# Performance work log

Measured on AMD Instinct MI355X. Metric: run time of the kernel, lower is better.

The kernel has to match this reference:

```python
import jax, jax.numpy as jnp
import numpy as np

N_ATOMS = 8192
N_EDGES = 262144
N_MOL = 128
F = 128
R = 20
CUTOFF = 5.0
L = 3
EPS = 1e-8


def setup_inputs() -> dict:
    key = jax.random.key(0)
    ks = jax.random.split(key, 20)
    sc = 0.05  # weight init scale for numerical stability
    inp = {
        "z": jax.random.randint(ks[0], (N_ATOMS,), 0, 100, dtype=jnp.int32),
        "pos": jax.random.uniform(ks[1], (N_ATOMS, 3), dtype=jnp.float32),
        "edge_src": jax.random.randint(ks[2], (N_EDGES,), 0, N_ATOMS, dtype=jnp.int32),
        "edge_dst": jax.random.randint(ks[3], (N_EDGES,), 0, N_ATOMS, dtype=jnp.int32),
        "mol_idx": jnp.sort(jax.random.randint(ks[4], (N_ATOMS,), 0, N_MOL, dtype=jnp.int32)),
        "embed": jax.random.normal(ks[5], (100, F), dtype=jnp.float32) * sc,
        "msg_w1": jax.random.normal(ks[6], (L, F, F), dtype=jnp.float32) * sc,
        "msg_b1": jnp.zeros((L, F), jnp.float32),
        "msg_w2": jax.random.normal(ks[7], (L, F, 3 * F), dtype=jnp.float32) * sc,
        "msg_b2": jnp.zeros((L, 3 * F), jnp.float32),
        "rbf_w": jax.random.normal(ks[8], (L, R, 3 * F), dtype=jnp.float32) * sc,
        "rbf_b": jnp.zeros((L, 3 * F), jnp.float32),
        "upd_u": jax.random.normal(ks[9], (L, F, F), dtype=jnp.float32) * sc,
        "upd_v": jax.random.normal(ks[10], (L, F, F), dtype=jnp.float32) * sc,
        "upd_a1": jax.random.normal(ks[11], (L, 2 * F, F), dtype=jnp.float32) * sc,
        "upd_a1b": jnp.zeros((L, F), jnp.float32),
        "upd_a2": jax.random.normal(ks[12], (L, F, 3 * F), dtype=jnp.float32) * sc,
        "upd_a2b": jnp.zeros((L, 3 * F), jnp.float32),
        "out_w1": jax.random.normal(ks[13], (F, F), dtype=jnp.float32) * sc,
        "out_b1": jnp.zeros((F,), jnp.float32),
        "out_w2": jax.random.normal(ks[14], (F, 1), dtype=jnp.float32) * sc,
        "out_b2": jnp.zeros((1,), jnp.float32),
    }
    return inp


def _painn_forward(z, pos, edge_src, edge_dst, mol_idx, embed,
                   msg_w1, msg_b1, msg_w2, msg_b2, rbf_w, rbf_b,
                   upd_u, upd_v, upd_a1, upd_a1b, upd_a2, upd_a2b,
                   out_w1, out_b1, out_w2, out_b2):
    n = z.shape[0]
    s = embed[z]                                  # [N,F]
    v = jnp.zeros((n, 3, F), s.dtype)             # [N,3,F]

    rij = pos[edge_dst] - pos[edge_src]           # [E,3]
    d = jnp.sqrt(jnp.sum(rij * rij, axis=-1) + EPS)  # [E]
    unit = rij / d[:, None]                       # [E,3]
    freq = jnp.arange(1, R + 1, dtype=s.dtype) * (jnp.pi / CUTOFF)
    rbf = jnp.sin(d[:, None] * freq[None, :]) / d[:, None]          # [E,R]
    fc = 0.5 * (jnp.cos(jnp.pi * d / CUTOFF) + 1.0) * (d < CUTOFF)  # [E]

    for l in range(L):
        # --- message block ---
        phi = jax.nn.silu(s @ msg_w1[l] + msg_b1[l]) @ msg_w2[l] + msg_b2[l]  # [N,3F]
        wfilt = (rbf @ rbf_w[l] + rbf_b[l]) * fc[:, None]                      # [E,3F]
        m = phi[edge_src] * wfilt                                              # [E,3F]
        ds_e, dvv, dvs = m[:, :F], m[:, F:2 * F], m[:, 2 * F:]
        ds = jax.ops.segment_sum(ds_e, edge_dst, num_segments=n)
        dv_e = v[edge_src] * dvv[:, None, :] + unit[:, :, None] * dvs[:, None, :]  # [E,3,F]
        dv = jax.ops.segment_sum(dv_e, edge_dst, num_segments=n)
        s = s + ds
        v = v + dv
        # --- update block ---
        uv = jnp.einsum('ncf,fg->ncg', v, upd_u[l])   # [N,3,F]
        vv = jnp.einsum('ncf,fg->ncg', v, upd_v[l])   # [N,3,F]
        vv_norm = jnp.sqrt(jnp.sum(vv * vv, axis=1) + EPS)  # [N,F]
        a = jax.nn.silu(jnp.concatenate([s, vv_norm], axis=-1) @ upd_a1[l] + upd_a1b[l])
        a = a @ upd_a2[l] + upd_a2b[l]                # [N,3F]
        a_vv, a_sv, a_ss = a[:, :F], a[:, F:2 * F], a[:, 2 * F:]
        s = s + a_ss + a_sv * jnp.sum(uv * vv, axis=1)
        v = v + a_vv[:, None, :] * uv

    atom_out = jax.nn.silu(s @ out_w1 + out_b1) @ out_w2 + out_b2  # [N,1]
    return jax.ops.segment_sum(atom_out, mol_idx, num_segments=N_MOL)  # [M,1]


def reference(z, pos, edge_src, edge_dst, mol_idx, embed,
              msg_w1, msg_b1, msg_w2, msg_b2, rbf_w, rbf_b,
              upd_u, upd_v, upd_a1, upd_a1b, upd_a2, upd_a2b,
              out_w1, out_b1, out_w2, out_b2):
    return _painn_forward(z, pos, edge_src, edge_dst, mol_idx, embed,
                          msg_w1, msg_b1, msg_w2, msg_b2, rbf_w, rbf_b,
                          upd_u, upd_v, upd_a1, upd_a1b, upd_a2, upd_a2b,
                          out_w1, out_b1, out_w2, out_b2)
```

## Files before the change

### kernel.cpp

```cpp
#include <hip/hip_runtime.h>
#include <hip/hip_bf16.h>
#include <math.h>

#define N_ATOMS 8192
#define N_EDGES 262144
#define N_MOL   128
#define FDIM    128
#define RDIM    20
#define LLAYERS 3
#define CUTOFF  5.0f
#define EPSV    1e-8f
#define PI_F    3.14159265358979323846f

typedef __attribute__((ext_vector_type(8))) short bf16x8;
typedef __attribute__((ext_vector_type(4))) float f32x4;

#define VPLANE 1048576

__device__ __forceinline__ ushort f2bf(float x) {
    uint b = __float_as_uint(x);
    return (ushort)((b + 0x7fffu + ((b >> 16) & 1u)) >> 16);
}

__global__ void k_wconv(const float* __restrict__ w1, const float* __restrict__ w2,
                        const float* __restrict__ uu, const float* __restrict__ uvw,
                        const float* __restrict__ a1, const float* __restrict__ a2,
                        const float* __restrict__ ow1, ushort* __restrict__ WT) {
    int i = blockIdx.x * 256 + threadIdx.x;
    float v;
    if (i < 49152) {
        int idx = i; int l = idx >> 14; idx &= 16383;
        int n = idx >> 7, k = idx & 127;
        v = w1[l*16384 + k*128 + n];
    } else if (i < 196608) {
        int idx = i - 49152; int l = idx / 49152; idx -= l * 49152;
        int n = idx >> 7, k = idx & 127;
        v = w2[l*49152 + k*384 + n];
    } else if (i < 294912) {
        int idx = i - 196608; int l = idx >> 15; idx &= 32767;
        int n = idx >> 7, k = idx & 127;
        v = (n < 128) ? uu[l*16384 + k*128 + n] : uvw[l*16384 + k*128 + (n-128)];
    } else if (i < 393216) {
        int idx = i - 294912; int l = idx >> 15; idx &= 32767;
        int n = idx >> 8, k = idx & 255;
        v = a1[l*32768 + k*128 + n];
    } else if (i < 540672) {
        int idx = i - 393216; int l = idx / 49152; idx -= l * 49152;
        int n = idx >> 7, k = idx & 127;
        v = a2[l*49152 + k*384 + n];
    } else {
        int idx = i - 540672;
        int n = idx >> 7, k = idx & 127;
        v = ow1[k*128 + n];
    }
    WT[i] = f2bf(v);
}

__global__ void k_embed(const int* __restrict__ z, const float* __restrict__ embed,
                        float* __restrict__ S, ushort* __restrict__ SBF) {
    int i = blockIdx.x * 256 + threadIdx.x;
    int a = i >> 7, k = i & 127;
    float v = embed[(size_t)z[a] * FDIM + k];
    S[i] = v; SBF[i] = f2bf(v);
}

__global__ void k_hist(const int* __restrict__ edst, int* __restrict__ CNT) {
    int e = blockIdx.x * 256 + threadIdx.x;
    if (e < N_EDGES) atomicAdd(&CNT[edst[e]], 1);
}

__global__ __launch_bounds__(1024) void k_scan(const int* __restrict__ CNT,
                                               int* __restrict__ OFF, int* __restrict__ CUR) {
    __shared__ int part[1024];
    int t = threadIdx.x;
    int loc[8];
    int run = 0;
    #pragma unroll
    for (int i = 0; i < 8; i++) { int c = CNT[t*8 + i]; loc[i] = run; run += c; }
    part[t] = run;
    __syncthreads();
    for (int off = 1; off < 1024; off <<= 1) {
        int v = 0;
        if (t >= off) v = part[t - off];
        __syncthreads();
        part[t] += v;
        __syncthreads();
    }
    int ebase = (t > 0) ? part[t-1] : 0;
    #pragma unroll
    for (int i = 0; i < 8; i++) { int o = ebase + loc[i]; OFF[t*8+i] = o; CUR[t*8+i] = o; }
    if (t == 1023) OFF[8192] = part[1023];
}

__global__ void k_edges(const float* __restrict__ pos, const int* __restrict__ esrc,
                        const int* __restrict__ edst, int* __restrict__ CUR,
                        float* __restrict__ UNITFC, int* __restrict__ SRCS) {
    int e = blockIdx.x * 256 + threadIdx.x;
    if (e >= N_EDGES) return;
    int s = esrc[e], d = edst[e];
    int p = atomicAdd(&CUR[d], 1);
    float rx = pos[d*3+0] - pos[s*3+0];
    float ry = pos[d*3+1] - pos[s*3+1];
    float rz = pos[d*3+2] - pos[s*3+2];
    float dd = sqrtf(rx*rx + ry*ry + rz*rz + EPSV);
    float inv = 1.0f / dd;
    float4 u4; u4.x = rx*inv; u4.y = ry*inv; u4.z = rz*inv; u4.w = dd;
    *(float4*)&UNITFC[(size_t)p*4] = u4;
    SRCS[p] = s;
}

__global__ __launch_bounds__(256) void k_msg(
    const ushort* __restrict__ SBF, const ushort* __restrict__ W1T, const float* __restrict__ b1,
    const ushort* __restrict__ W2T, const float* __restrict__ b2, ushort* __restrict__ PHIB)
{
    int tid = threadIdx.x;
    int w = tid >> 6, l = tid & 63;
    int bm = blockIdx.x * 16;
    int lrow = l & 15, lk = (l >> 4) * 8;
    __shared__ ushort Hs[16][136];

    f32x4 acc[2] = {{0.f,0.f,0.f,0.f},{0.f,0.f,0.f,0.f}};
    #pragma unroll
    for (int k0 = 0; k0 < 128; k0 += 32) {
        bf16x8 af = *(const bf16x8*)&SBF[(size_t)(bm + lrow)*128 + k0 + lk];
        #pragma unroll
        for (int t = 0; t < 2; t++) {
            int n = (2*w + t)*16 + lrow;
            bf16x8 bf = *(const bf16x8*)&W1T[(size_t)n*128 + k0 + lk];
            acc[t] = __builtin_amdgcn_mfma_f32_16x16x32_bf16(af, bf, acc[t], 0, 0, 0);
        }
    }
    #pragma unroll
    for (int t = 0; t < 2; t++) {
        int col = (2*w + t)*16 + lrow;
        float bv = b1[col];
        #pragma unroll
        for (int j = 0; j < 4; j++) {
            int row = (l >> 4)*4 + j;
            float val = acc[t][j] + bv;
            val = val / (1.0f + __expf(-val));
            Hs[row][col] = f2bf(val);
        }
    }
    __syncthreads();

    f32x4 acc2[6];
    #pragma unroll
    for (int t = 0; t < 6; t++) acc2[t] = (f32x4){0.f,0.f,0.f,0.f};
    #pragma unroll
    for (int k0 = 0; k0 < 128; k0 += 32) {
        bf16x8 af = *(const bf16x8*)&Hs[lrow][k0 + lk];
        #pragma unroll
        for (int t = 0; t < 6; t++) {
            int n = (6*w + t)*16 + lrow;
            bf16x8 bf = *(const bf16x8*)&W2T[(size_t)n*128 + k0 + lk];
            acc2[t] = __builtin_amdgcn_mfma_f32_16x16x32_bf16(af, bf, acc2[t], 0, 0, 0);
        }
    }
    #pragma unroll
    for (int t = 0; t < 6; t++) {
        int col = (6*w + t)*16 + lrow;
        float bv = b2[col];
        #pragma unroll
        for (int j = 0; j < 4; j++) {
            int row = bm + (l >> 4)*4 + j;
            PHIB[(size_t)row*384 + col] = f2bf(acc2[t][j] + bv);
        }
    }
}

template<bool L0>
__global__ __launch_bounds__(192) void k_aggregate(
    const ushort* __restrict__ PHIB, const ushort* __restrict__ VBFA,
    float* __restrict__ S, ushort* __restrict__ SBF,
    float* __restrict__ V, ushort* __restrict__ VBFB,
    const float* __restrict__ UNITFC,
    const int* __restrict__ SRCS, const int* __restrict__ OFF,
    const float* __restrict__ rbfw, const float* __restrict__ rbfb)
{
    int a = blockIdx.x;
    int tid = threadIdx.x;
    int g = tid >> 6;
    int c0 = 2 * (tid & 63);

    float2 w[RDIM];
    const float* wc = rbfw + g*128 + c0;
    #pragma unroll
    for (int r = 0; r < RDIM; r++) { w[r].x = wc[r*384]; w[r].y = wc[r*384 + 1]; }
    float2 bb; bb.x = rbfb[g*128 + c0]; bb.y = rbfb[g*128 + c0 + 1];

    __shared__ int sSrc[64];
    __shared__ float4 sRBF[320];
    __shared__ float4 sUFC[64];
    __shared__ float avs[3][128];
    float* sRBFf = (float*)sRBF;

    int beg = OFF[a], end = OFF[a + 1];
    float2 d; d.x = 0.f; d.y = 0.f;
    float2 A0, A1, A2v;
    A0.x=A0.y=A1.x=A1.y=A2v.x=A2v.y=0.f;

    for (int p0 = beg; p0 < end; p0 += 64) {
        int n = end - p0; if (n > 64) n = 64;
        __syncthreads();
        if (tid < n) {
            sSrc[tid] = SRCS[p0 + tid];
            float4 u4 = *(const float4*)(UNITFC + (size_t)(p0 + tid) * 4);
            float dd = u4.w;
            u4.w = (dd < CUTOFF) ? 0.5f * (__cosf(dd * (PI_F / CUTOFF)) + 1.0f) : 0.0f;
            sUFC[tid] = u4;
        }
        for (int i = tid; i < n * RDIM; i += 192) {
            int e = i / RDIM, r = i - e * RDIM;
            float dd = UNITFC[(size_t)(p0 + e) * 4 + 3];
            sRBFf[i] = __sinf(dd * (float)(r + 1) * (PI_F / CUTOFF)) / dd;
        }
        __syncthreads();

        if (L0 && g == 1) continue;

        uint phA[4], u0A[4], u1A[4], u2A[4];
        uint phB[4], u0B[4], u1B[4], u2B[4];

        auto grpLoad = [&](int base, uint* ph, uint* u0, uint* u1, uint* u2) {
            #pragma unroll
            for (int j = 0; j < 4; j++) {
                int q = base + j;
                int src = sSrc[(q < n) ? q : 0];
                size_t pb = (size_t)src * 128;
                ph[j] = *(const uint*)&PHIB[(size_t)src*384 + g*128 + c0];
                if (!L0 && g == 1) {
                    u0[j] = *(const uint*)&VBFA[pb + c0];
                    u1[j] = *(const uint*)&VBFA[pb + VPLANE + c0];
                    u2[j] = *(const uint*)&VBFA[pb + 2*VPLANE + c0];
                }
            }
        };
        grpLoad(0, phA, u0A, u1A, u2A);
        for (int q0 = 0; q0 < n; q0 += 4) {
            if (q0 + 4 < n) grpLoad(q0 + 4, phB, u0B, u1B, u2B);
            #pragma unroll
            for (int j = 0; j < 4; j++) {
                int q = q0 + j;
                if (q >= n) break;
                float4 r0 = sRBF[q*5+0], r1 = sRBF[q*5+1], r2 = sRBF[q*5+2],
                       r3 = sRBF[q*5+3], r4 = sRBF[q*5+4];
                float4 ufc = sUFC[q];
                float2 f = bb;
                f.x += r0.x*w[0].x;   f.y += r0.x*w[0].y;
                f.x += r0.y*w[1].x;   f.y += r0.y*w[1].y;
                f.x += r0.z*w[2].x;   f.y += r0.z*w[2].y;
                f.x += r0.w*w[3].x;   f.y += r0.w*w[3].y;
                f.x += r1.x*w[4].x;   f.y += r1.x*w[4].y;
                f.x += r1.y*w[5].x;   f.y += r1.y*w[5].y;
                f.x += r1.z*w[6].x;   f.y += r1.z*w[6].y;
                f.x += r1.w*w[7].x;   f.y += r1.w*w[7].y;
                f.x += r2.x*w[8].x;   f.y += r2.x*w[8].y;
                f.x += r2.y*w[9].x;   f.y += r2.y*w[9].y;
                f.x += r2.z*w[10].x;  f.y += r2.z*w[10].y;
                f.x += r2.w*w[11].x;  f.y += r2.w*w[11].y;
                f.x += r3.x*w[12].x;  f.y += r3.x*w[12].y;
                f.x += r3.y*w[13].x;  f.y += r3.y*w[13].y;
                f.x += r3.z*w[14].x;  f.y += r3.z*w[14].y;
                f.x += r3.w*w[15].x;  f.y += r3.w*w[15].y;
                f.x += r4.x*w[16].x;  f.y += r4.x*w[16].y;
                f.x += r4.y*w[17].x;  f.y += r4.y*w[17].y;
                f.x += r4.z*w[18].x;  f.y += r4.z*w[18].y;
                f.x += r4.w*w[19].x;  f.y += r4.w*w[19].y;
                uint up = phA[j];
                float m0 = __uint_as_float(up << 16)         * (f.x * ufc.w);
                float m1 = __uint_as_float(up & 0xffff0000u) * (f.y * ufc.w);
                if (g == 0) {
                    d.x += m0; d.y += m1;
                } else if (g == 1) {
                    A0.x  += __uint_as_float(u0A[j] << 16)         * m0;
                    A0.y  += __uint_as_float(u0A[j] & 0xffff0000u) * m1;
                    A1.x  += __uint_as_float(u1A[j] << 16)         * m0;
                    A1.y  += __uint_as_float(u1A[j] & 0xffff0000u) * m1;
                    A2v.x += __uint_as_float(u2A[j] << 16)         * m0;
                    A2v.y += __uint_as_float(u2A[j] & 0xffff0000u) * m1;
                } else {
                    A0.x  += ufc.x * m0; A0.y  += ufc.x * m1;
                    A1.x  += ufc.y * m0; A1.y  += ufc.y * m1;
                    A2v.x += ufc.z * m0; A2v.y += ufc.z * m1;
                }
            }
            #pragma unroll
            for (int j = 0; j < 4; j++) {
                phA[j] = phB[j]; u0A[j] = u0B[j]; u1A[j] = u1B[j]; u2A[j] = u2B[j];
            }
        }
    }

    if (g == 1) {
        avs[0][c0] = A0.x;  avs[0][c0+1] = A0.y;
        avs[1][c0] = A1.x;  avs[1][c0+1] = A1.y;
        avs[2][c0] = A2v.x; avs[2][c0+1] = A2v.y;
    }
    __syncthreads();
    if (g == 0) {
        size_t sb = (size_t)a*128 + c0;
        float2 s2 = *(float2*)&S[sb];
        s2.x += d.x; s2.y += d.y;
        *(float2*)&S[sb] = s2;
        SBF[sb] = f2bf(s2.x); SBF[sb+1] = f2bf(s2.y);
    } else if (g == 2) {
        float own0[3] = {A0.x, A1.x, A2v.x};
        float own1[3] = {A0.y, A1.y, A2v.y};
        #pragma unroll
        for (int c = 0; c < 3; c++) {
            size_t vb = (size_t)c*VPLANE + (size_t)a*128 + c0;
            float2 vi;
            if (L0) { vi.x = 0.f; vi.y = 0.f; }
            else    vi = *(const float2*)&V[vb];
            vi.x += avs[c][c0]     + own0[c];
            vi.y += avs[c][c0 + 1] + own1[c];
            *(float2*)&V[vb] = vi;
            VBFB[vb] = f2bf(vi.x); VBFB[vb+1] = f2bf(vi.y);
        }
    }
}

__global__ __launch_bounds__(256) void k_upd(
    const ushort* __restrict__ VBFB, const ushort* __restrict__ UVT,
    const ushort* __restrict__ SBF_in,
    const ushort* __restrict__ A1T, const float* __restrict__ a1b,
    const ushort* __restrict__ A2T, const float* __restrict__ a2b,
    float* __restrict__ S, ushort* __restrict__ SBF,
    float* __restrict__ V, ushort* __restrict__ VBFA)
{
    int tid = threadIdx.x;
    int w = tid >> 6, l = tid & 63;
    int bm = blockIdx.x * 16;
    int lrow = l & 15, lk = (l >> 4) * 8;
    __shared__ ushort sVVN[16][136];
    __shared__ ushort Hs[16][136];

    f32x4 au[3][2], av[3][2];
    #pragma unroll
    for (int c = 0; c < 3; c++)
        #pragma unroll
        for (int t = 0; t < 2; t++) {
            au[c][t] = (f32x4){0.f,0.f,0.f,0.f};
            av[c][t] = (f32x4){0.f,0.f,0.f,0.f};
        }
    #pragma unroll
    for (int k0 = 0; k0 < 128; k0 += 32) {
        bf16x8 af[3];
        #pragma unroll
        for (int c = 0; c < 3; c++)
            af[c] = *(const bf16x8*)&VBFB[(size_t)c*VPLANE + (size_t)(bm + lrow)*128 + k0 + lk];
        #pragma unroll
        for (int t = 0; t < 2; t++) {
            int nu = (2*w + t)*16 + lrow;
            bf16x8 bu = *(const bf16x8*)&UVT[(size_t)nu*128 + k0 + lk];
            bf16x8 bv = *(const bf16x8*)&UVT[(size_t)(nu + 128)*128 + k0 + lk];
            #pragma unroll
            for (int c = 0; c < 3; c++) {
                au[c][t] = __builtin_amdgcn_mfma_f32_16x16x32_bf16(af[c], bu, au[c][t], 0, 0, 0);
                av[c][t] = __builtin_amdgcn_mfma_f32_16x16x32_bf16(af[c], bv, av[c][t], 0, 0, 0);
            }
        }
    }
    float dotr[2][4], uvr[3][2][4];
    #pragma unroll
    for (int t = 0; t < 2; t++) {
        int k = (2*w + t)*16 + lrow;
        #pragma unroll
        for (int j = 0; j < 4; j++) {
            int row = (l >> 4)*4 + j;
            float u0 = au[0][t][j], u1 = au[1][t][j], u2 = au[2][t][j];
            float v0 = av[0][t][j], v1 = av[1][t][j], v2 = av[2][t][j];
            uvr[0][t][j] = u0; uvr[1][t][j] = u1; uvr[2][t][j] = u2;
            dotr[t][j] = u0*v0 + u1*v1 + u2*v2;
            sVVN[row][k] = f2bf(sqrtf(v0*v0 + v1*v1 + v2*v2 + EPSV));
        }
    }
    __syncthreads();

    f32x4 acc[2] = {{0.f,0.f,0.f,0.f},{0.f,0.f,0.f,0.f}};
    #pragma unroll
    for (int k0 = 0; k0 < 256; k0 += 32) {
        bf16x8 af;
        if (k0 < 128) af = *(const bf16x8*)&SBF_in[(size_t)(bm + lrow)*128 + k0 + lk];
        else          af = *(const bf16x8*)&sVVN[lrow][k0 + lk - 128];
        #pragma unroll
        for (int t = 0; t < 2; t++) {
            int n = (2*w + t)*16 + lrow;
            bf16x8 bf = *(const bf16x8*)&A1T[(size_t)n*256 + k0 + lk];
            acc[t] = __builtin_amdgcn_mfma_f32_16x16x32_bf16(af, bf, acc[t], 0, 0, 0);
        }
    }
    #pragma unroll
    for (int t = 0; t < 2; t++) {
        int col = (2*w + t)*16 + lrow;
        float bv = a1b[col];
        #pragma unroll
        for (int j = 0; j < 4; j++) {
            int row = (l >> 4)*4 + j;
            float val = acc[t][j] + bv;
            val = val / (1.0f + __expf(-val));
            Hs[row][col] = f2bf(val);
        }
    }
    __syncthreads();

    f32x4 c_vv[2], c_sv[2], c_ss[2];
    #pragma unroll
    for (int t = 0; t < 2; t++) {
        c_vv[t] = (f32x4){0.f,0.f,0.f,0.f};
        c_sv[t] = (f32x4){0.f,0.f,0.f,0.f};
        c_ss[t] = (f32x4){0.f,0.f,0.f,0.f};
    }
    #pragma unroll
    for (int k0 = 0; k0 < 128; k0 += 32) {
        bf16x8 af = *(const bf16x8*)&Hs[lrow][k0 + lk];
        #pragma unroll
        for (int t = 0; t < 2; t++) {
            int n0 = (2*w + t)*16 + lrow;
            bf16x8 b0 = *(const bf16x8*)&A2T[(size_t)n0*128 + k0 + lk];
            bf16x8 b1 = *(const bf16x8*)&A2T[(size_t)(n0 + 128)*128 + k0 + lk];
            bf16x8 b2 = *(const bf16x8*)&A2T[(size_t)(n0 + 256)*128 + k0 + lk];
            c_vv[t] = __builtin_amdgcn_mfma_f32_16x16x32_bf16(af, b0, c_vv[t], 0, 0, 0);
            c_sv[t] = __builtin_amdgcn_mfma_f32_16x16x32_bf16(af, b1, c_sv[t], 0, 0, 0);
            c_ss[t] = __builtin_amdgcn_mfma_f32_16x16x32_bf16(af, b2, c_ss[t], 0, 0, 0);
        }
    }
    #pragma unroll
    for (int t = 0; t < 2; t++) {
        int k = (2*w + t)*16 + lrow;
        float b_vv = a2b[k], b_sv = a2b[128 + k], b_ss = a2b[256 + k];
        #pragma unroll
        for (int j = 0; j < 4; j++) {
            int a = bm + (l >> 4)*4 + j;
            size_t base = (size_t)a*128 + k;
            float vv = c_vv[t][j] + b_vv;
            float sv = c_sv[t][j] + b_sv;
            float ss = c_ss[t][j] + b_ss;
            float sn = S[base] + ss + sv * dotr[t][j];
            S[base] = sn; SBF[base] = f2bf(sn);
            #pragma unroll
            for (int c = 0; c < 3; c++) {
                size_t vb = (size_t)c*VPLANE + base;
                float nv = V[vb] + vv * uvr[c][t][j];
                V[vb] = nv; VBFA[vb] = f2bf(nv);
            }
        }
    }
}

__global__ __launch_bounds__(64) void k_readout(
    const ushort* __restrict__ SBF, const ushort* __restrict__ OW1T,
    const float* __restrict__ b1, const float* __restrict__ w2,
    const float* __restrict__ b2v, const int* __restrict__ mol,
    float* __restrict__ out)
{
    int l = threadIdx.x;
    int bm = blockIdx.x * 16;
    int lrow = l & 15, lk = (l >> 4) * 8;
    __shared__ float Hs[16][132];

    f32x4 acc[8];
    #pragma unroll
    for (int t = 0; t < 8; t++) acc[t] = (f32x4){0.f,0.f,0.f,0.f};
    #pragma unroll
    for (int k0 = 0; k0 < 128; k0 += 32) {
        bf16x8 af = *(const bf16x8*)&SBF[(size_t)(bm + lrow)*128 + k0 + lk];
        #pragma unroll
        for (int t = 0; t < 8; t++) {
            bf16x8 bf = *(const bf16x8*)&OW1T[(size_t)(t*16 + lrow)*128 + k0 + lk];
            acc[t] = __builtin_amdgcn_mfma_f32_16x16x32_bf16(af, bf, acc[t], 0, 0, 0);
        }
    }
    #pragma unroll
    for (int t = 0; t < 8; t++) {
        int col = t*16 + lrow;
        float bv = b1[col];
        #pragma unroll
        for (int j = 0; j < 4; j++) {
            int row = (l >> 4)*4 + j;
            float val = acc[t][j] + bv;
            Hs[row][col] = val / (1.0f + __expf(-val));
        }
    }
    __syncthreads();
    if (l < 16) {
        float s = b2v[0];
        #pragma unroll 8
        for (int k = 0; k < 128; k++) s += Hs[l][k] * w2[k];
        atomicAdd(&out[mol[bm + l]], s);
    }
}

extern "C" void kernel_launch(void* const* d_in, const int* in_sizes, int n_in,
                              void* d_out, int out_size, void* d_ws, size_t ws_size,
                              hipStream_t stream) {
    const int*   z      = (const int*)d_in[0];
    const float* pos    = (const float*)d_in[1];
    const int*   esrc   = (const int*)d_in[2];
    const int*   edst   = (const int*)d_in[3];
    const int*   mol    = (const int*)d_in[4];
    const float* embed  = (const float*)d_in[5];
    const float* msg_w1 = (const float*)d_in[6];
    const float* msg_b1 = (const float*)d_in[7];
    const float* msg_w2 = (const float*)d_in[8];
    const float* msg_b2 = (const float*)d_in[9];
    const float* rbf_w  = (const float*)d_in[10];
    const float* rbf_b  = (const float*)d_in[11];
    const float* upd_u  = (const float*)d_in[12];
    const float* upd_v  = (const float*)d_in[13];
    const float* upd_a1 = (const float*)d_in[14];
    const float* upd_a1b= (const float*)d_in[15];
    const float* upd_a2 = (const float*)d_in[16];
    const float* upd_a2b= (const float*)d_in[17];
    const float* out_w1 = (const float*)d_in[18];
    const float* out_b1 = (const float*)d_in[19];
    const float* out_w2 = (const float*)d_in[20];
    const float* out_b2 = (const float*)d_in[21];

    float* ws = (float*)d_ws;
    float* S      = ws; ws += 1048576;
    float* V      = ws; ws += 3145728;
    float* UNITFC = ws; ws += 1048576;
    ushort* PHIB  = (ushort*)ws; ws += 1572864;
    ushort* VBFA  = (ushort*)ws; ws += 1572864;
    ushort* VBFB  = (ushort*)ws; ws += 1572864;
    ushort* SBF   = (ushort*)ws; ws += 524288;
    ushort* WT    = (ushort*)ws; ws += 278528;
    int* CNT  = (int*)ws;
    int* OFF  = CNT + 8192;
    int* CUR  = OFF + 8193;
    int* SRCS = CUR + 8192;

    hipMemsetAsync(CNT, 0, 8192 * sizeof(int), stream);
    hipMemsetAsync(d_out, 0, N_MOL * sizeof(float), stream);

    k_wconv<<<2176, 256, 0, stream>>>(msg_w1, msg_w2, upd_u, upd_v, upd_a1, upd_a2, out_w1, WT);
    k_embed<<<4096, 256, 0, stream>>>(z, embed, S, SBF);
    k_hist<<<1024, 256, 0, stream>>>(edst, CNT);
    k_scan<<<1, 1024, 0, stream>>>(CNT, OFF, CUR);
    k_edges<<<1024, 256, 0, stream>>>(pos, esrc, edst, CUR, UNITFC, SRCS);

    for (int l = 0; l < LLAYERS; l++) {
        const ushort* W1T = WT + l*16384;
        const ushort* W2T = WT + 49152  + l*49152;
        const ushort* UVT = WT + 196608 + l*32768;
        const ushort* A1T = WT + 294912 + l*32768;
        const ushort* A2T = WT + 393216 + l*49152;

        k_msg<<<512, 256, 0, stream>>>(SBF, W1T, msg_b1 + (size_t)l*128,
                                       W2T, msg_b2 + (size_t)l*384, PHIB);
        if (l == 0)
            k_aggregate<true><<<8192, 192, 0, stream>>>(PHIB, VBFA, S, SBF, V, VBFB,
                UNITFC, SRCS, OFF, rbf_w + (size_t)l*20*384, rbf_b + (size_t)l*384);
        else
            k_aggregate<false><<<8192, 192, 0, stream>>>(PHIB, VBFA, S, SBF, V, VBFB,
                UNITFC, SRCS, OFF, rbf_w + (size_t)l*20*384, rbf_b + (size_t)l*384);
        k_upd<<<512, 256, 0, stream>>>(VBFB, UVT, SBF, A1T, upd_a1b + (size_t)l*128,
            A2T, upd_a2b + (size_t)l*384, S, SBF, V, VBFA);
    }

    k_readout<<<512, 64, 0, stream>>>(SBF, WT + 540672, out_b1, out_w2, out_b2,
                                      mol, (float*)d_out);
}
```

Measured before the change: 603.1 us.

## Fuse next-layer message MLP into update kernel and skip final vector update

The update kernel now optionally computes the next layer's message MLP (two bf16 MFMA GEMMs with SiLU) on its freshly updated scalar tile held in shared memory, writing PHIB directly. This removes two separate k_msg launches and the re-read of SBF from global memory. The last layer's update also skips writing V and its bf16 copy, since nothing reads them afterward. The cost is extra register and LDS pressure inside k_upd, which may lower occupancy.

Result: faster. 586.5 us (-2.8%).

```diff
diff --git a/kernel.cpp b/kernel.cpp
--- a/kernel.cpp
+++ b/kernel.cpp
@@ -321,13 +321,17 @@
     }
 }
 
+template<bool FUSE_MSG, bool LAST>
 __global__ __launch_bounds__(256) void k_upd(
     const ushort* __restrict__ VBFB, const ushort* __restrict__ UVT,
     const ushort* __restrict__ SBF_in,
     const ushort* __restrict__ A1T, const float* __restrict__ a1b,
     const ushort* __restrict__ A2T, const float* __restrict__ a2b,
     float* __restrict__ S, ushort* __restrict__ SBF,
-    float* __restrict__ V, ushort* __restrict__ VBFA)
+    float* __restrict__ V, ushort* __restrict__ VBFA,
+    const ushort* __restrict__ W1Tn, const float* __restrict__ b1n,
+    const ushort* __restrict__ W2Tn, const float* __restrict__ b2n,
+    ushort* __restrict__ PHIB)
 {
     int tid = threadIdx.x;
     int w = tid >> 6, l = tid & 63;
@@ -439,11 +443,65 @@
             float ss = c_ss[t][j] + b_ss;
             float sn = S[base] + ss + sv * dotr[t][j];
             S[base] = sn; SBF[base] = f2bf(sn);
-            #pragma unroll
-            for (int c = 0; c < 3; c++) {
-                size_t vb = (size_t)c*VPLANE + base;
-                float nv = V[vb] + vv * uvr[c][t][j];
-                V[vb] = nv; VBFA[vb] = f2bf(nv);
+            if (FUSE_MSG) sVVN[a - bm][k] = f2bf(sn);
+            if (!LAST) {
+                #pragma unroll
+                for (int c = 0; c < 3; c++) {
+                    size_t vb = (size_t)c*VPLANE + base;
+                    float nv = V[vb] + vv * uvr[c][t][j];
+                    V[vb] = nv; VBFA[vb] = f2bf(nv);
+                }
+            }
+        }
+    }
+
+    if (FUSE_MSG) {
+        __syncthreads();
+        f32x4 accD[2] = {{0.f,0.f,0.f,0.f},{0.f,0.f,0.f,0.f}};
+        #pragma unroll
+        for (int k0 = 0; k0 < 128; k0 += 32) {
+            bf16x8 af = *(const bf16x8*)&sVVN[lrow][k0 + lk];
+            #pragma unroll
+            for (int t = 0; t < 2; t++) {
+                int n = (2*w + t)*16 + lrow;
+                bf16x8 bf = *(const bf16x8*)&W1Tn[(size_t)n*128 + k0 + lk];
+                accD[t] = __builtin_amdgcn_mfma_f32_16x16x32_bf16(af, bf, accD[t], 0, 0, 0);
+            }
+        }
+        #pragma unroll
+        for (int t = 0; t < 2; t++) {
+            int col = (2*w + t)*16 + lrow;
+            float bv = b1n[col];
+            #pragma unroll
+            for (int j = 0; j < 4; j++) {
+                int row = (l >> 4)*4 + j;
+                float val = accD[t][j] + bv;
+                val = val / (1.0f + __expf(-val));
+                Hs[row][col] = f2bf(val);
+            }
+        }
+        __syncthreads();
+        f32x4 accE[6];
+        #pragma unroll
+        for (int t = 0; t < 6; t++) accE[t] = (f32x4){0.f,0.f,0.f,0.f};
+        #pragma unroll
+        for (int k0 = 0; k0 < 128; k0 += 32) {
+            bf16x8 af = *(const bf16x8*)&Hs[lrow][k0 + lk];
+            #pragma unroll
+            for (int t = 0; t < 6; t++) {
+                int n = (6*w + t)*16 + lrow;
+                bf16x8 bf = *(const bf16x8*)&W2Tn[(size_t)n*128 + k0 + lk];
+                accE[t] = __builtin_amdgcn_mfma_f32_16x16x32_bf16(af, bf, accE[t], 0, 0, 0);
+            }
+        }
+        #pragma unroll
+        for (int t = 0; t < 6; t++) {
+            int col = (6*w + t)*16 + lrow;
+            float bv = b2n[col];
+            #pragma unroll
+            for (int j = 0; j < 4; j++) {
+                int row = bm + (l >> 4)*4 + j;
+                PHIB[(size_t)row*384 + col] = f2bf(accE[t][j] + bv);
             }
         }
     }
@@ -541,24 +599,30 @@
     k_scan<<<1, 1024, 0, stream>>>(CNT, OFF, CUR);
     k_edges<<<1024, 256, 0, stream>>>(pos, esrc, edst, CUR, UNITFC, SRCS);
 
-    for (int l = 0; l < LLAYERS; l++) {
-        const ushort* W1T = WT + l*16384;
-        const ushort* W2T = WT + 49152  + l*49152;
-        const ushort* UVT = WT + 196608 + l*32768;
-        const ushort* A1T = WT + 294912 + l*32768;
-        const ushort* A2T = WT + 393216 + l*49152;
-
-        k_msg<<<512, 256, 0, stream>>>(SBF, W1T, msg_b1 + (size_t)l*128,
-                                       W2T, msg_b2 + (size_t)l*384, PHIB);
-        if (l == 0)
-            k_aggregate<true><<<8192, 192, 0, stream>>>(PHIB, VBFA, S, SBF, V, VBFB,
-                UNITFC, SRCS, OFF, rbf_w + (size_t)l*20*384, rbf_b + (size_t)l*384);
-        else
-            k_aggregate<false><<<8192, 192, 0, stream>>>(PHIB, VBFA, S, SBF, V, VBFB,
-                UNITFC, SRCS, OFF, rbf_w + (size_t)l*20*384, rbf_b + (size_t)l*384);
-        k_upd<<<512, 256, 0, stream>>>(VBFB, UVT, SBF, A1T, upd_a1b + (size_t)l*128,
-            A2T, upd_a2b + (size_t)l*384, S, SBF, V, VBFA);
-    }
+    const ushort* W1T0 = WT;
+    const ushort* W2T0 = WT + 49152;
+    auto UVTl = [&](int l){ return WT + 196608 + l*32768; };
+    auto A1Tl = [&](int l){ return WT + 294912 + l*32768; };
+    auto A2Tl = [&](int l){ return WT + 393216 + l*49152; };
+    auto W1Tl = [&](int l){ return WT + l*16384; };
+    auto W2Tl = [&](int l){ return WT + 49152 + l*49152; };
+
+    k_msg<<<512, 256, 0, stream>>>(SBF, W1T0, msg_b1, W2T0, msg_b2, PHIB);
+    k_aggregate<true><<<8192, 192, 0, stream>>>(PHIB, VBFA, S, SBF, V, VBFB,
+        UNITFC, SRCS, OFF, rbf_w, rbf_b);
+    k_upd<true,false><<<512, 256, 0, stream>>>(VBFB, UVTl(0), SBF, A1Tl(0), upd_a1b,
+        A2Tl(0), upd_a2b, S, SBF, V, VBFA,
+        W1Tl(1), msg_b1 + 128, W2Tl(1), msg_b2 + 384, PHIB);
+    k_aggregate<false><<<8192, 192, 0, stream>>>(PHIB, VBFA, S, SBF, V, VBFB,
+        UNITFC, SRCS, OFF, rbf_w + (size_t)1*20*384, rbf_b + 384);
+    k_upd<true,false><<<512, 256, 0, stream>>>(VBFB, UVTl(1), SBF, A1Tl(1), upd_a1b + 128,
+        A2Tl(1), upd_a2b + 384, S, SBF, V, VBFA,
+        W1Tl(2), msg_b1 + 256, W2Tl(2), msg_b2 + 768, PHIB);
+    k_aggregate<false><<<8192, 192, 0, stream>>>(PHIB, VBFA, S, SBF, V, VBFB,
+        UNITFC, SRCS, OFF, rbf_w + (size_t)2*20*384, rbf_b + 768);
+    k_upd<false,true><<<512, 256, 0, stream>>>(VBFB, UVTl(2), SBF, A1Tl(2), upd_a1b + 256,
+        A2Tl(2), upd_a2b + 768, S, SBF, V, VBFA,
+        nullptr, nullptr, nullptr, nullptr, nullptr);
 
     k_readout<<<512, 64, 0, stream>>>(SBF, WT + 540672, out_b1, out_w2, out_b2,
                                       mol, (float*)d_out);
```
